# Optimization experiments

Measured on AMD Instinct MI355X. Metric: run time of the kernel, lower is better.

Reference implementation:

```python
import jax, jax.numpy as jnp
import numpy as np

D_HEAD = 128
N_HEADS = 8
BATCH = 8
SEQ = 1024


def setup_inputs() -> dict:
    key = jax.random.key(0)
    ks = jax.random.split(key, 11)
    d, nh = D_HEAD, N_HEADS
    D = nh * d
    s_in = 1.0 / np.sqrt(d)   # torch Linear default init bound, fan_in=d
    s_out = 1.0 / np.sqrt(D)  # fan_in=D for out_proj
    u = lambda k, shape, s: jax.random.uniform(k, shape, jnp.float32, -s, s)
    return {
        "q": jax.random.normal(ks[0], (BATCH, SEQ, d), jnp.float32),
        "k": jax.random.normal(ks[1], (BATCH, SEQ, d), jnp.float32),
        "v": jax.random.normal(ks[2], (BATCH, SEQ, d), jnp.float32),
        "Wq": u(ks[3], (d, D), s_in), "bq": u(ks[4], (D,), s_in),
        "Wk": u(ks[5], (d, D), s_in), "bk": u(ks[6], (D,), s_in),
        "Wv": u(ks[7], (d, D), s_in), "bv": u(ks[8], (D,), s_in),
        "Wo": u(ks[9], (D, d), s_out), "bo": u(ks[10], (d,), s_out),
    }


def reference(q, k, v, Wq, bq, Wk, bk, Wv, bv, Wo, bo):
    B, T, d_in = q.shape
    S = k.shape[1]
    nh = N_HEADS
    # projections: [B, L, nh*d] -> [B, nh, L, d]
    split = lambda x: x.reshape(x.shape[0], x.shape[1], nh, -1).transpose(0, 2, 1, 3)
    qh = split(q @ Wq + bq)
    kh = split(k @ Wk + bk)
    vh = split(v @ Wv + bv)
    d_head = qh.shape[-1]
    # scaled dot-product scores: [B, nh, T, S]
    scores = jnp.einsum('bhtd,bhsd->bhts', qh, kh) / jnp.sqrt(jnp.float32(d_head))
    # causal mask (future positions -> -inf), matches triu(fill(-inf), 1)
    causal = jnp.triu(jnp.ones((T, S), dtype=bool), 1)
    scores = jnp.where(causal[None, None], -jnp.inf, scores)
    # softmax in float32 then cast back, as the original does
    probs = jax.nn.softmax(scores.astype(jnp.float32), axis=-1).astype(scores.dtype)
    o = jnp.einsum('bhts,bhsd->bhtd', probs, vh)          # [B, nh, T, d]
    o = o.transpose(0, 2, 1, 3).reshape(B, T, nh * d_head)  # [B, T, D]
    return o @ Wo + bo                                     # [B, T, d]
```

## Files before the change

kernel.cpp:

```cpp
#include <hip/hip_runtime.h>
#include <hip/hip_bf16.h>


typedef __attribute__((ext_vector_type(8))) short short8;
typedef __attribute__((ext_vector_type(4))) short short4v;
typedef __attribute__((ext_vector_type(4))) float f32x4;

#define B_   8
#define S_   1024
#define DH_  128
#define NH_  8
#define DM_  1024

#define MFMA16(a, b, c) __builtin_amdgcn_mfma_f32_16x16x32_bf16((a), (b), (c), 0, 0, 0)

#define GLOAD_LDS16(gsrc, ldst)                                              \
  __builtin_amdgcn_global_load_lds(                                          \
      (const __attribute__((address_space(1))) void*)(gsrc),                 \
      (__attribute__((address_space(3))) void*)(ldst), 16, 0, 0)

__device__ __forceinline__ float bf2f(unsigned short u) {
  union { unsigned int i; float f; } x; x.i = ((unsigned int)u) << 16; return x.f;
}
__device__ __forceinline__ unsigned short f2bf(float f) {
  union { float f; unsigned int i; } x; x.f = f;
  unsigned int r = (x.i + 0x7fffu + ((x.i >> 16) & 1u)) >> 16;
  return (unsigned short)r;
}
__device__ __forceinline__ unsigned short f2h(float f) {
  union { _Float16 h; unsigned short u; } x; x.h = (_Float16)f; return x.u;
}
__device__ __forceinline__ float h2f(unsigned short u) {
  union { unsigned short u; _Float16 h; } x; x.u = u; return (float)x.h;
}
__device__ __forceinline__ float ldany(const void* p, int i, int fp) {
  return fp ? ((const float*)p)[i] : bf2f(((const unsigned short*)p)[i]);
}

__global__ void k_detect(const unsigned short* __restrict__ in, int* __restrict__ flag) {
  __shared__ int f;
  int tid = threadIdx.x;
  if (tid == 0) f = 0;
  __syncthreads();
  int t = 0;
  for (int i = tid; i < 16384; i += 256) {
    unsigned h = in[i];
    unsigned e = (h >> 7) & 0xFFu, m = h & 0x7Fu;
    if (e == 0xFFu || (e == 0u && m != 0u)) t = 1;
  }
  if (t) atomicOr(&f, 1);
  __syncthreads();
  if (tid == 0) *flag = f;
}

__global__ void k_cvt(const void* __restrict__ q, const void* __restrict__ k,
                      const void* __restrict__ v,
                      const void* __restrict__ Wq, const void* __restrict__ Wk,
                      const void* __restrict__ Wv, const void* __restrict__ Wo,
                      const void* __restrict__ bq, const void* __restrict__ bk,
                      const void* __restrict__ bv, const void* __restrict__ bo,
                      const int* __restrict__ flag,
                      unsigned short* __restrict__ Xq, unsigned short* __restrict__ Xk,
                      unsigned short* __restrict__ Xv,
                      unsigned short* __restrict__ wqT, unsigned short* __restrict__ wkT,
                      unsigned short* __restrict__ wvT, unsigned short* __restrict__ woT,
                      unsigned short* __restrict__ bqc, unsigned short* __restrict__ bkc,
                      unsigned short* __restrict__ bvc, unsigned short* __restrict__ boc) {
  const int fp = *flag;
  if (blockIdx.x < 1536) {
    int z = blockIdx.x / 512, blk = blockIdx.x % 512;
    const void* in = (z == 0) ? q : (z == 1) ? k : v;
    unsigned short* out = (z == 0) ? Xq : (z == 1) ? Xk : Xv;
    int e8 = (blk * 256 + threadIdx.x) * 8;
    if (fp) {
      const float* xf = (const float*)in + e8;
      f32x4 x0 = *(const f32x4*)xf;
      f32x4 x1 = *(const f32x4*)(xf + 4);
      short8 o;
#pragma unroll
      for (int j = 0; j < 4; ++j) { o[j] = (short)f2bf(x0[j]); o[4 + j] = (short)f2bf(x1[j]); }
      *(short8*)&out[e8] = o;
    } else {
      *(short8*)&out[e8] = *(const short8*)((const unsigned short*)in + e8);
    }
    return;
  }
  int g = (blockIdx.x - 1536) * 256 + threadIdx.x;
  if (g < 393216) {
    int z = g >> 17, e = g & 131071;
    const void* in = (z == 0) ? Wq : (z == 1) ? Wk : Wv;
    unsigned short* out = (z == 0) ? wqT : (z == 1) ? wkT : wvT;
    int r = e >> 10, c = e & 1023;
    out[c * 128 + r] = f2bf(ldany(in, e, fp));
  } else if (g < 524288) {
    int e = g - 393216;
    int r = e >> 7, c = e & 127;
    woT[c * 1024 + r] = f2bf(ldany(Wo, e, fp));
  } else if (g < 525312) {
    int e = g - 524288; bqc[e] = f2bf(ldany(bq, e, fp));
  } else if (g < 526336) {
    int e = g - 525312; bkc[e] = f2bf(ldany(bk, e, fp));
  } else if (g < 527360) {
    int e = g - 526336; bvc[e] = f2bf(ldany(bv, e, fp));
  } else if (g < 527488) {
    int e = g - 527360; boc[e] = f2bf(ldany(bo, e, fp));
  }
}

__global__ __launch_bounds__(256) void k_qkv(
    const unsigned short* __restrict__ Xq, const unsigned short* __restrict__ Xk,
    const unsigned short* __restrict__ Xv,
    const unsigned short* __restrict__ WqT, const unsigned short* __restrict__ WkT,
    const unsigned short* __restrict__ WvT,
    const unsigned short* __restrict__ bq, const unsigned short* __restrict__ bk,
    const unsigned short* __restrict__ bv,
    unsigned short* __restrict__ Qp, unsigned short* __restrict__ Kp,
    unsigned short* __restrict__ VpT) {
  __shared__ __align__(16) unsigned short vtile[128][136];

  const int mat = blockIdx.z;
  const unsigned short* X    = (mat == 0) ? Xq  : (mat == 1) ? Xk  : Xv;
  const unsigned short* WT   = (mat == 0) ? WqT : (mat == 1) ? WkT : WvT;
  const unsigned short* bias = (mat == 0) ? bq  : (mat == 1) ? bk  : bv;
  const float scale = (mat == 0) ? (1.4426950408889634f / 11.313708498984761f) : 1.0f;

  const int tid = threadIdx.x, lane = tid & 63, wave = tid >> 6;
  const int wm = wave >> 1, wn = wave & 1;
  const int l15 = lane & 15, lg = lane >> 4;
  const int mbase = blockIdx.x * 128 + wm * 64;
  const int nbase = blockIdx.y * 128 + wn * 64;

  short8 a[4][4];
#pragma unroll
  for (int mi = 0; mi < 4; ++mi)
#pragma unroll
    for (int kk = 0; kk < 4; ++kk)
      a[mi][kk] = *(const short8*)&X[(mbase + mi * 16 + l15) * DH_ + kk * 32 + lg * 8];

  f32x4 acc[4][4];
#pragma unroll
  for (int mi = 0; mi < 4; ++mi)
#pragma unroll
    for (int ni = 0; ni < 4; ++ni) acc[mi][ni] = (f32x4){0.f, 0.f, 0.f, 0.f};

  short8 bfr[2][4];
#pragma unroll
  for (int kk = 0; kk < 4; ++kk)
    bfr[0][kk] = *(const short8*)&WT[(nbase + l15) * DH_ + kk * 32 + lg * 8];

#pragma unroll
  for (int ni = 0; ni < 4; ++ni) {
    if (ni < 3) {
#pragma unroll
      for (int kk = 0; kk < 4; ++kk)
        bfr[(ni + 1) & 1][kk] =
            *(const short8*)&WT[(nbase + (ni + 1) * 16 + l15) * DH_ + kk * 32 + lg * 8];
    }
#pragma unroll
    for (int mi = 0; mi < 4; ++mi)
#pragma unroll
      for (int kk = 0; kk < 4; ++kk)
        acc[mi][ni] = MFMA16(a[mi][kk], bfr[ni & 1][kk], acc[mi][ni]);
  }

#pragma unroll
  for (int mi = 0; mi < 4; ++mi)
#pragma unroll
    for (int ni = 0; ni < 4; ++ni) {
      int nl = wn * 64 + ni * 16 + l15;
      float bv_ = bf2f(bias[blockIdx.y * 128 + nl]);
#pragma unroll
      for (int reg = 0; reg < 4; ++reg) {
        int ml_ = wm * 64 + mi * 16 + lg * 4 + reg;
        vtile[ml_][nl] = f2bf((acc[mi][ni][reg] + bv_) * scale);
      }
    }
  __syncthreads();

  const int b = blockIdx.x >> 3;
  const int h = blockIdx.y;
  if (mat < 2) {
    unsigned short* Out = ((mat == 0) ? Qp : Kp) +
        ((b * NH_ + h) * S_ + (blockIdx.x & 7) * 128) * DH_;
#pragma unroll
    for (int j = 0; j < 8; ++j) {
      int r = j * 16 + (tid >> 4);
      int c0 = (tid & 15) * 8;
      short8 v = *(const short8*)&vtile[r][c0];
      *(short8*)&Out[j * 2048 + tid * 8] = v;
    }
  } else {
    int n = tid >> 1;
    int thalf = (tid & 1) * 64;
    int base = ((b * NH_ + h) * DH_ + n) * S_ + (blockIdx.x & 7) * 128 + thalf;
#pragma unroll
    for (int jj = 0; jj < 8; ++jj) {
      short8 v;
#pragma unroll
      for (int j2 = 0; j2 < 8; ++j2) v[j2] = (short)vtile[thalf + jj * 8 + j2][n];
      *(short8*)&VpT[base + jj * 8] = v;
    }
  }
}

__global__ __launch_bounds__(256) void k_attn_split(
    const unsigned short* __restrict__ Qp, const unsigned short* __restrict__ Kp,
    const unsigned short* __restrict__ VpT,
    unsigned short* __restrict__ Opart, float* __restrict__ ml,
    unsigned short* __restrict__ O) {
  __shared__ __align__(16) unsigned short kbuf[2][4096];
  __shared__ __align__(16) unsigned short vbuf[2][4096];
  __shared__ __align__(16) unsigned short plds[4][16][44];

  const int tid = threadIdx.x, lane = tid & 63, w = tid >> 6;
  const int l15 = lane & 15, lg = lane >> 4;

  const int bid = blockIdx.x;
  const int swz = (bid & 7) * 320 + (bid >> 3);
  const int bh = swz / 40;
  const int bj = 39 - (swz % 40);
  int G, c;
  if (bj < 4)       { G = bj;                  c = 0; }
  else if (bj < 12) { G = 4 + ((bj - 4) >> 1); c = (bj - 4) & 1; }
  else if (bj < 24) { G = 8 + (bj - 12) / 3;   c = (bj - 12) % 3; }
  else              { G = 12 + ((bj - 24) >> 2); c = (bj - 24) & 3; }
  const int qw = 4 * G + w;
  const int q0 = qw * 16;
  const int cd = G >> 2;
  const bool dia = (c == cd);
  const int sbeg = c * 256;
  const int nt_w   = dia ? ((qw >> 1) + 1 - 8 * c) : 8;
  const int nt_blk = dia ? (2 * G + 2 - 8 * c) : 8;

  const unsigned short* Qb = Qp + bh * (S_ * DH_);
  const unsigned short* Kb = Kp + bh * (S_ * DH_);
  const unsigned short* Vb = VpT + bh * (DH_ * S_);

  const int krow4 = lane >> 4;
  const int kslot = lane & 15;
  const int vd16  = lane >> 2;
  const int vslot = lane & 3;
  const int vsw   = vslot ^ ((vd16 >> 1) & 3);

#define STAGE(bb, sb_) do {                                                        \
    int r0_ = w * 8 + krow4;                                                       \
    GLOAD_LDS16(Kb + ((sb_) + r0_) * DH_ + ((kslot ^ (r0_ & 7)) * 8),              \
                &kbuf[bb][(w * 8) * 128]);                                         \
    int r1_ = w * 8 + 4 + krow4;                                                   \
    GLOAD_LDS16(Kb + ((sb_) + r1_) * DH_ + ((kslot ^ (r1_ & 7)) * 8),              \
                &kbuf[bb][(w * 8 + 4) * 128]);                                     \
    int d0_ = w * 32 + vd16;                                                       \
    GLOAD_LDS16(Vb + d0_ * S_ + (sb_) + vsw * 8, &vbuf[bb][(w * 32) * 32]);        \
    int d1_ = w * 32 + 16 + vd16;                                                  \
    GLOAD_LDS16(Vb + d1_ * S_ + (sb_) + vsw * 8, &vbuf[bb][(w * 32 + 16) * 32]);   \
  } while (0)

  short8 qf[4];
#pragma unroll
  for (int kk = 0; kk < 4; ++kk)
    qf[kk] = *(const short8*)&Qb[(q0 + l15) * DH_ + kk * 32 + lg * 8];

  short8 ones;
#pragma unroll
  for (int jj = 0; jj < 8; ++jj) ones[jj] = (short)0x3F80;

  f32x4 of[8], l_acc;
  float m_[4];
#pragma unroll
  for (int di = 0; di < 8; ++di) of[di] = (f32x4){0.f, 0.f, 0.f, 0.f};
  l_acc = (f32x4){0.f, 0.f, 0.f, 0.f};
#pragma unroll
  for (int reg = 0; reg < 4; ++reg) m_[reg] = -1e30f;

  STAGE(0, sbeg);
  __syncthreads();

  const int vrd = lg ^ ((l15 >> 1) & 3);
  for (int kt = 0; kt < nt_blk; ++kt) {
    const int cb = kt & 1;
    if (kt + 1 < nt_blk) STAGE(cb ^ 1, sbeg + (kt + 1) * 32);

    if (kt < nt_w) {
      const int sb = sbeg + kt * 32;
      const int xsl = l15 & 7;

      f32x4 s0 = (f32x4){0.f, 0.f, 0.f, 0.f}, s1 = (f32x4){0.f, 0.f, 0.f, 0.f};
#pragma unroll
      for (int kk = 0; kk < 4; ++kk) {
        short8 kf0 = *(const short8*)&kbuf[cb][l15 * 128 + (((kk * 4 + lg) ^ xsl) * 8)];
        short8 kf1 = *(const short8*)&kbuf[cb][(16 + l15) * 128 + (((kk * 4 + lg) ^ xsl) * 8)];
        s0 = MFMA16(qf[kk], kf0, s0);
        s1 = MFMA16(qf[kk], kf1, s1);
      }

      if (dia && kt == nt_w - 1) {
        const int qrow = q0 + lg * 4;
#pragma unroll
        for (int reg = 0; reg < 4; ++reg) {
          if (sb + l15 > qrow + reg)      s0[reg] = -1e30f;
          if (sb + 16 + l15 > qrow + reg) s1[reg] = -1e30f;
        }
      }

      bool need = false;
      float vmax[4];
#pragma unroll
      for (int reg = 0; reg < 4; ++reg) {
        vmax[reg] = fmaxf(s0[reg], s1[reg]);
        need |= (vmax[reg] > m_[reg] + 8.0f);
      }
      if (__any(need)) {
        float alpha[4];
#pragma unroll
        for (int reg = 0; reg < 4; ++reg) {
          float rm = vmax[reg];
#pragma unroll
          for (int d = 1; d < 16; d <<= 1) rm = fmaxf(rm, __shfl_xor(rm, d));
          float mn = fmaxf(m_[reg], rm);
          alpha[reg] = __builtin_amdgcn_exp2f(m_[reg] - mn);
          m_[reg] = mn;
        }
#pragma unroll
        for (int di = 0; di < 8; ++di)
#pragma unroll
          for (int reg = 0; reg < 4; ++reg) of[di][reg] *= alpha[reg];
#pragma unroll
        for (int reg = 0; reg < 4; ++reg) l_acc[reg] *= alpha[reg];
      }

#pragma unroll
      for (int reg = 0; reg < 4; ++reg) {
        float p0 = __builtin_amdgcn_exp2f(s0[reg] - m_[reg]);
        float p1 = __builtin_amdgcn_exp2f(s1[reg] - m_[reg]);
        union { float f; unsigned int i; } u0, u1;
        u0.f = p0; u1.f = p1;
        plds[w][lg * 4 + reg][l15]      = (unsigned short)((u0.i + 0x8000u) >> 16);
        plds[w][lg * 4 + reg][16 + l15] = (unsigned short)((u1.i + 0x8000u) >> 16);
      }

      short8 pa = *(const short8*)&plds[w][l15][lg * 8];

#pragma unroll
      for (int di = 0; di < 8; ++di) {
        short8 vfd = *(const short8*)&vbuf[cb][(di * 16 + l15) * 32 + vrd * 8];
        of[di] = MFMA16(pa, vfd, of[di]);
      }
      l_acc = MFMA16(pa, ones, l_acc);
    }
    __syncthreads();
  }

  if (qw < 16) {
    const int b = bh >> 3, h = bh & 7;
#pragma unroll
    for (int reg = 0; reg < 4; ++reg) {
      int row = lg * 4 + reg;
      float inv = 1.0f / l_acc[reg];
      int qq = q0 + row;
#pragma unroll
      for (int di = 0; di < 8; ++di)
        O[(b * S_ + qq) * DM_ + h * DH_ + di * 16 + l15] = f2bf(of[di][reg] * inv);
    }
  } else {
    int runit;
    if (qw < 32)      runit = 16 + 2 * (qw - 16) + c;
    else if (qw < 48) runit = 48 + 3 * (qw - 32) + c;
    else              runit = 96 + 4 * (qw - 48) + c;
    const int g = bh * 160 + runit;
    unsigned short* op = Opart + g * 2048;
    float* mlg = ml + g * 32;
#pragma unroll
    for (int reg = 0; reg < 4; ++reg) {
      int row = lg * 4 + reg;
      float inv = 1.0f / l_acc[reg];
#pragma unroll
      for (int di = 0; di < 8; ++di)
        op[row * 128 + di * 16 + l15] = f2h(of[di][reg] * inv);
      if (l15 == 0) {
        mlg[row * 2]     = m_[reg];
        mlg[row * 2 + 1] = l_acc[reg];
      }
    }
  }
#undef STAGE
}

__global__ void k_combine(const unsigned short* __restrict__ Opart,
                          const float* __restrict__ ml,
                          unsigned short* __restrict__ O) {
  const int bh = blockIdx.x / 48, qw = 16 + blockIdx.x % 48;
  const int nc = (qw >> 4) + 1;
  const int rbase = (qw < 32) ? 16 + 2 * (qw - 16)
                  : (qw < 48) ? 48 + 3 * (qw - 32)
                              : 96 + 4 * (qw - 48);
  const int g0 = bh * 160 + rbase;
  const int tid = threadIdx.x;
  const int row = tid >> 4, d0 = (tid & 15) * 8;

  float m[4], l[4];
  float mx = -1e30f;
  for (int i = 0; i < nc; ++i) {
    m[i] = ml[(g0 + i) * 32 + row * 2];
    l[i] = ml[(g0 + i) * 32 + row * 2 + 1];
    mx = fmaxf(mx, m[i]);
  }
  float wt[4], wsum = 0.f;
  for (int i = 0; i < nc; ++i) { wt[i] = l[i] * exp2f(m[i] - mx); wsum += wt[i]; }
  float invw = 1.0f / wsum;

  float acc[8];
#pragma unroll
  for (int jj = 0; jj < 8; ++jj) acc[jj] = 0.f;
  for (int i = 0; i < nc; ++i) {
    short8 v = *(const short8*)&Opart[(g0 + i) * 2048 + row * 128 + d0];
    float wgt = wt[i];
#pragma unroll
    for (int jj = 0; jj < 8; ++jj) acc[jj] += wgt * h2f((unsigned short)v[jj]);
  }

  const int b = bh >> 3, h = bh & 7;
  const int qq = qw * 16 + row;
  short8 o;
#pragma unroll
  for (int jj = 0; jj < 8; ++jj) o[jj] = (short)f2bf(acc[jj] * invw);
  *(short8*)&O[(b * S_ + qq) * DM_ + h * DH_ + d0] = o;
}

__global__ __launch_bounds__(256) void k_attn(
    const unsigned short* __restrict__ Qp, const unsigned short* __restrict__ Kp,
    const unsigned short* __restrict__ VpT, unsigned short* __restrict__ O) {
  __shared__ __align__(16) unsigned short plds[4][2][16][44];

  const int qt = 7 - blockIdx.x;
  const int bh = blockIdx.y;
  const int tid = threadIdx.x, lane = tid & 63, w = tid >> 6;
  const int l15 = lane & 15, lg = lane >> 4;
  const int q0 = qt * 128 + w * 32;

  const unsigned short* Qb = Qp + bh * (S_ * DH_);
  const unsigned short* Kb = Kp + bh * (S_ * DH_);
  const unsigned short* Vb = VpT + bh * (DH_ * S_);

  short8 qf[2][4];
#pragma unroll
  for (int mi = 0; mi < 2; ++mi)
#pragma unroll
    for (int kk = 0; kk < 4; ++kk)
      qf[mi][kk] = *(const short8*)&Qb[(q0 + mi * 16 + l15) * DH_ + kk * 32 + lg * 8];

  f32x4 of[2][8];
  float m_[2][4], l_[2][4];
#pragma unroll
  for (int mi = 0; mi < 2; ++mi) {
#pragma unroll
    for (int di = 0; di < 8; ++di) of[mi][di] = (f32x4){0.f, 0.f, 0.f, 0.f};
#pragma unroll
    for (int reg = 0; reg < 4; ++reg) { m_[mi][reg] = -1e30f; l_[mi][reg] = 0.f; }
  }

  const int ntiles = q0 / 32 + 1;
  for (int kt = 0; kt < ntiles; ++kt) {
    const int sb = kt * 32;
    const bool lastt = (kt == ntiles - 1);

    f32x4 s[2][2];
#pragma unroll
    for (int mi = 0; mi < 2; ++mi)
#pragma unroll
      for (int ni = 0; ni < 2; ++ni) s[mi][ni] = (f32x4){0.f, 0.f, 0.f, 0.f};
#pragma unroll
    for (int ni = 0; ni < 2; ++ni) {
      short8 kf[4];
#pragma unroll
      for (int kk = 0; kk < 4; ++kk)
        kf[kk] = *(const short8*)&Kb[(sb + ni * 16 + l15) * DH_ + kk * 32 + lg * 8];
#pragma unroll
      for (int mi = 0; mi < 2; ++mi)
#pragma unroll
        for (int kk = 0; kk < 4; ++kk)
          s[mi][ni] = MFMA16(qf[mi][kk], kf[kk], s[mi][ni]);
    }

#pragma unroll
    for (int mi = 0; mi < 2; ++mi) {
      float alpha[4];
#pragma unroll
      for (int reg = 0; reg < 4; ++reg) {
        int q = q0 + mi * 16 + lg * 4 + reg;
        float v0 = s[mi][0][reg];
        float v1 = s[mi][1][reg];
        if (lastt) {
          if (sb + l15 > q)      v0 = -1e30f;
          if (sb + 16 + l15 > q) v1 = -1e30f;
        }
        float rmax = fmaxf(v0, v1);
#pragma unroll
        for (int d = 1; d < 16; d <<= 1) rmax = fmaxf(rmax, __shfl_xor(rmax, d));
        float mn = fmaxf(m_[mi][reg], rmax);
        alpha[reg] = __builtin_amdgcn_exp2f(m_[mi][reg] - mn);
        m_[mi][reg] = mn;
        float p0 = __builtin_amdgcn_exp2f(v0 - mn), p1 = __builtin_amdgcn_exp2f(v1 - mn);
        float rs = p0 + p1;
#pragma unroll
        for (int d = 1; d < 16; d <<= 1) rs += __shfl_xor(rs, d);
        l_[mi][reg] = l_[mi][reg] * alpha[reg] + rs;
        plds[w][mi][lg * 4 + reg][l15]      = f2bf(p0);
        plds[w][mi][lg * 4 + reg][16 + l15] = f2bf(p1);
      }
#pragma unroll
      for (int di = 0; di < 8; ++di)
#pragma unroll
        for (int reg = 0; reg < 4; ++reg) of[mi][di][reg] *= alpha[reg];
    }

    short8 pa[2];
#pragma unroll
    for (int mi = 0; mi < 2; ++mi)
      pa[mi] = *(const short8*)&plds[w][mi][l15][lg * 8];

#pragma unroll
    for (int di = 0; di < 8; ++di) {
      short8 vf = *(const short8*)&Vb[(di * 16 + l15) * S_ + sb + lg * 8];
#pragma unroll
      for (int mi = 0; mi < 2; ++mi) of[mi][di] = MFMA16(pa[mi], vf, of[mi][di]);
    }
  }

  const int b = bh >> 3, h = bh & 7;
#pragma unroll
  for (int mi = 0; mi < 2; ++mi)
#pragma unroll
    for (int reg = 0; reg < 4; ++reg) {
      float inv = 1.0f / l_[mi][reg];
      int q = q0 + mi * 16 + lg * 4 + reg;
#pragma unroll
      for (int di = 0; di < 8; ++di) {
        int d = di * 16 + l15;
        O[(b * S_ + q) * DM_ + h * DH_ + d] = f2bf(of[mi][di][reg] * inv);
      }
    }
}

__global__ __launch_bounds__(256) void k_oproj(
    const unsigned short* __restrict__ O, const unsigned short* __restrict__ WoT,
    float* __restrict__ outacc) {
  const int tid = threadIdx.x, lane = tid & 63, wave = tid >> 6;
  const int wm = wave >> 1, wn = wave & 1;
  const int l15 = lane & 15, lg = lane >> 4;
  const int mbase = blockIdx.x * 128 + wm * 64;
  const int kc = blockIdx.y;

  f32x4 acc[4][4];
#pragma unroll
  for (int mi = 0; mi < 4; ++mi)
#pragma unroll
    for (int ni = 0; ni < 4; ++ni) acc[mi][ni] = (f32x4){0.f, 0.f, 0.f, 0.f};

  short8 a[2][4], bfr[2][4];
  {
    int kb = kc * 256;
#pragma unroll
    for (int mi = 0; mi < 4; ++mi)
      a[0][mi] = *(const short8*)&O[(mbase + mi * 16 + l15) * DM_ + kb + lg * 8];
#pragma unroll
    for (int ni = 0; ni < 4; ++ni)
      bfr[0][ni] = *(const short8*)&WoT[(wn * 64 + ni * 16 + l15) * DM_ + kb + lg * 8];
  }

#pragma unroll
  for (int ks = 0; ks < 8; ++ks) {
    const int cur = ks & 1;
    if (ks < 7) {
      int kb = kc * 256 + (ks + 1) * 32;
#pragma unroll
      for (int mi = 0; mi < 4; ++mi)
        a[cur ^ 1][mi] = *(const short8*)&O[(mbase + mi * 16 + l15) * DM_ + kb + lg * 8];
#pragma unroll
      for (int ni = 0; ni < 4; ++ni)
        bfr[cur ^ 1][ni] = *(const short8*)&WoT[(wn * 64 + ni * 16 + l15) * DM_ + kb + lg * 8];
    }
#pragma unroll
    for (int mi = 0; mi < 4; ++mi)
#pragma unroll
      for (int ni = 0; ni < 4; ++ni)
        acc[mi][ni] = MFMA16(a[cur][mi], bfr[cur][ni], acc[mi][ni]);
  }

  float* oa = outacc + kc * (8192 * 128);
#pragma unroll
  for (int mi = 0; mi < 4; ++mi)
#pragma unroll
    for (int ni = 0; ni < 4; ++ni) {
      int n = wn * 64 + ni * 16 + l15;
#pragma unroll
      for (int reg = 0; reg < 4; ++reg) {
        int m = mbase + mi * 16 + lg * 4 + reg;
        oa[m * 128 + n] = acc[mi][ni][reg];
      }
    }
}

__global__ void k_final(const float* __restrict__ outacc,
                        const unsigned short* __restrict__ boc,
                        const int* __restrict__ flag, void* __restrict__ out) {
  int i4 = (blockIdx.x * 256 + threadIdx.x) * 4;
  f32x4 v = *(const f32x4*)&outacc[i4];
  v += *(const f32x4*)&outacc[1048576 + i4];
  v += *(const f32x4*)&outacc[2097152 + i4];
  v += *(const f32x4*)&outacc[3145728 + i4];
  int n0 = i4 & 127;
#pragma unroll
  for (int j = 0; j < 4; ++j) v[j] += bf2f(boc[n0 + j]);
  if (*flag) {
    *(f32x4*)&((float*)out)[i4] = v;
  } else {
    short4v o;
#pragma unroll
    for (int j = 0; j < 4; ++j) o[j] = (short)f2bf(v[j]);
    *(short4v*)&((unsigned short*)out)[i4] = o;
  }
}

extern "C" void kernel_launch(void* const* d_in, const int* in_sizes, int n_in,
                              void* d_out, int out_size, void* d_ws, size_t ws_size,
                              hipStream_t stream) {
  const void* q  = d_in[0];
  const void* k  = d_in[1];
  const void* v  = d_in[2];
  const void* Wq = d_in[3];
  const void* bq = d_in[4];
  const void* Wk = d_in[5];
  const void* bk = d_in[6];
  const void* Wv = d_in[7];
  const void* bv = d_in[8];
  const void* Wo = d_in[9];
  const void* bo = d_in[10];

  char* ws = (char*)d_ws;
  int*            flag = (int*)(ws + 0);
  unsigned short* wqT  = (unsigned short*)(ws + 4096);
  unsigned short* wkT  = (unsigned short*)(ws + 266240);
  unsigned short* wvT  = (unsigned short*)(ws + 528384);
  unsigned short* woT  = (unsigned short*)(ws + 790528);
  unsigned short* bqc  = (unsigned short*)(ws + 1052672);
  unsigned short* bkc  = (unsigned short*)(ws + 1054720);
  unsigned short* bvc  = (unsigned short*)(ws + 1056768);
  unsigned short* boc  = (unsigned short*)(ws + 1058816);
  unsigned short* Xq   = (unsigned short*)(ws + 2097152);
  unsigned short* Xk   = (unsigned short*)(ws + 4194304);
  unsigned short* Xv   = (unsigned short*)(ws + 6291456);
  float*          ml   = (float*)(ws + 2097152);
  unsigned short* Qp   = (unsigned short*)(ws + 8388608);
  unsigned short* Kp   = (unsigned short*)(ws + 25165824);
  unsigned short* VpT  = (unsigned short*)(ws + 41943040);
  unsigned short* O    = (unsigned short*)(ws + 58720256);
  unsigned short* Opart= (unsigned short*)(ws + 75497472);
  float*          oacc = (float*)(ws + 75497472);

  const bool use_split = ws_size >= (size_t)117440512;

  k_detect<<<dim3(1), 256, 0, stream>>>((const unsigned short*)q, flag);
  k_cvt<<<dim3(3597), 256, 0, stream>>>(q, k, v, Wq, Wk, Wv, Wo, bq, bk, bv, bo, flag,
                                        Xq, Xk, Xv, wqT, wkT, wvT, woT,
                                        bqc, bkc, bvc, boc);
  k_qkv<<<dim3(64, 8, 3), 256, 0, stream>>>(Xq, Xk, Xv, wqT, wkT, wvT, bqc, bkc, bvc,
                                            Qp, Kp, VpT);
  if (use_split) {
    k_attn_split<<<dim3(2560), 256, 0, stream>>>(Qp, Kp, VpT, Opart, ml, O);
    k_combine<<<dim3(3072), 256, 0, stream>>>(Opart, ml, O);
  } else {
    k_attn<<<dim3(8, 64), 256, 0, stream>>>(Qp, Kp, VpT, O);
  }
  k_oproj<<<dim3(64, 4), 256, 0, stream>>>(O, woT, oacc);
  k_final<<<dim3(1024), 256, 0, stream>>>(oacc, boc, flag, d_out);
}
```

Measured before the change: 140.9 us.

## Use 8-wave attention blocks so each K/V tile serves 128 query rows

Doubles the split-attention block to 512 threads (8 waves), so each block covers 128 query rows and every staged K/V tile is reused by twice as many waves. Each wave now issues one K load and one V load per tile instead of two each, and the grid is halved. The work-assignment table is rebuilt for the new group/chunk layout, putting heavy diagonal groups first. The trade-off is fewer, larger blocks, which may lower occupancy flexibility and leave causal-diagonal imbalance within a block, and the hidden kernel body must match the new wave count and indexing.

```diff
diff --git a/kernel.cpp b/kernel.cpp
--- a/kernel.cpp
+++ b/kernel.cpp
@@ -203,56 +203,56 @@
   }
 }
 
-__global__ __launch_bounds__(256) void k_attn_split(
+__global__ __launch_bounds__(512) void k_attn_split(
     const unsigned short* __restrict__ Qp, const unsigned short* __restrict__ Kp,
     const unsigned short* __restrict__ VpT,
     unsigned short* __restrict__ Opart, float* __restrict__ ml,
     unsigned short* __restrict__ O) {
   __shared__ __align__(16) unsigned short kbuf[2][4096];
   __shared__ __align__(16) unsigned short vbuf[2][4096];
-  __shared__ __align__(16) unsigned short plds[4][16][44];
+  __shared__ __align__(16) unsigned short plds[8][16][44];
 
   const int tid = threadIdx.x, lane = tid & 63, w = tid >> 6;
   const int l15 = lane & 15, lg = lane >> 4;
 
   const int bid = blockIdx.x;
-  const int swz = (bid & 7) * 320 + (bid >> 3);
-  const int bh = swz / 40;
-  const int bj = 39 - (swz % 40);
+  const int swz = (bid & 7) * 160 + (bid >> 3);
+  const int bh = swz / 20;
+  const int bj = swz % 20;
   int G, c;
-  if (bj < 4)       { G = bj;                  c = 0; }
-  else if (bj < 12) { G = 4 + ((bj - 4) >> 1); c = (bj - 4) & 1; }
-  else if (bj < 24) { G = 8 + (bj - 12) / 3;   c = (bj - 12) % 3; }
-  else              { G = 12 + ((bj - 24) >> 2); c = (bj - 24) & 3; }
-  const int qw = 4 * G + w;
+  if (bj < 4)        { G = 7; c = bj; }
+  else if (bj < 7)   { G = 6; c = bj - 4; }
+  else if (bj < 10)  { G = 5; c = bj - 7; }
+  else if (bj < 12)  { G = 4; c = bj - 10; }
+  else if (bj < 14)  { G = 3; c = bj - 12; }
+  else if (bj == 14) { G = 2; c = 0; }
+  else if (bj == 15) { G = 1; c = 0; }
+  else if (bj == 16) { G = 6; c = 3; }
+  else if (bj == 17) { G = 4; c = 2; }
+  else if (bj == 18) { G = 2; c = 1; }
+  else               { G = 0; c = 0; }
+  const int qw = 8 * G + w;
   const int q0 = qw * 16;
-  const int cd = G >> 2;
+  const int cd = G >> 1;
   const bool dia = (c == cd);
   const int sbeg = c * 256;
   const int nt_w   = dia ? ((qw >> 1) + 1 - 8 * c) : 8;
-  const int nt_blk = dia ? (2 * G + 2 - 8 * c) : 8;
+  const int nt_blk = dia ? (4 * G + 4 - 8 * c) : 8;
 
   const unsigned short* Qb = Qp + bh * (S_ * DH_);
   const unsigned short* Kb = Kp + bh * (S_ * DH_);
   const unsigned short* Vb = VpT + bh * (DH_ * S_);
 
-  const int krow4 = lane >> 4;
+  const int krow = w * 4 + (lane >> 4);
   const int kslot = lane & 15;
-  const int vd16  = lane >> 2;
+  const int vd   = w * 16 + (lane >> 2);
   const int vslot = lane & 3;
-  const int vsw   = vslot ^ ((vd16 >> 1) & 3);
+  const int vsw  = vslot ^ ((vd >> 1) & 3);
 
 #define STAGE(bb, sb_) do {                                                        \
-    int r0_ = w * 8 + krow4;                                                       \
-    GLOAD_LDS16(Kb + ((sb_) + r0_) * DH_ + ((kslot ^ (r0_ & 7)) * 8),              \
-                &kbuf[bb][(w * 8) * 128]);                                         \
-    int r1_ = w * 8 + 4 + krow4;                                                   \
-    GLOAD_LDS16(Kb + ((sb_) + r1_) * DH_ + ((kslot ^ (r1_ & 7)) * 8),              \
-                &kbuf[bb][(w * 8 + 4) * 128]);                                     \
-    int d0_ = w * 32 + vd16;                                                       \
-    GLOAD_LDS16(Vb + d0_ * S_ + (sb_) + vsw * 8, &vbuf[bb][(w * 32) * 32]);        \
-    int d1_ = w * 32 + 16 + vd16;                                                  \
-    GLOAD_LDS16(Vb + d1_ * S_ + (sb_) + vsw * 8, &vbuf[bb][(w * 32 + 16) * 32]);   \
+    GLOAD_LDS16(Kb + ((sb_) + krow) * DH_ + ((kslot ^ (krow & 7)) * 8),            \
+                &kbuf[bb][(w * 4) * 128]);                                         \
+    GLOAD_LDS16(Vb + vd * S_ + (sb_) + vsw * 8, &vbuf[bb][(w * 16) * 32]);         \
   } while (0)
 
   short8 qf[4];
@@ -666,7 +666,7 @@
   k_qkv<<<dim3(64, 8, 3), 256, 0, stream>>>(Xq, Xk, Xv, wqT, wkT, wvT, bqc, bkc, bvc,
                                             Qp, Kp, VpT);
   if (use_split) {
-    k_attn_split<<<dim3(2560), 256, 0, stream>>>(Qp, Kp, VpT, Opart, ml, O);
+    k_attn_split<<<dim3(1280), 512, 0, stream>>>(Qp, Kp, VpT, Opart, ml, O);
     k_combine<<<dim3(3072), 256, 0, stream>>>(Opart, ml, O);
   } else {
     k_attn<<<dim3(8, 64), 256, 0, stream>>>(Qp, Kp, VpT, O);
```

Measured after the change: 135.5 us, median of 3. 3.8% less time.
